# Kernel optimization log

Hardware: AMD Instinct MI355X
Metric: run time of the kernel (lower is better)

Reference implementation:

```python
import jax, jax.numpy as jnp
import numpy as np

D_MODEL = 1024
NUM_HEADS = 16
HEAD_DIM = D_MODEL // NUM_HEADS


def setup_inputs() -> dict:
    key = jax.random.key(0)
    k0, k1, k2, k3, k4 = jax.random.split(key, 5)
    B, S, D = 4, 2048, D_MODEL
    std = np.sqrt(2.0 / (D + D)).astype(np.float32)
    return {
        "in_features": jax.random.normal(k0, (B, S, D), dtype=jnp.float32),
        "Wq": jax.random.normal(k1, (D, D), dtype=jnp.float32) * std,
        "Wk": jax.random.normal(k2, (D, D), dtype=jnp.float32) * std,
        "Wv": jax.random.normal(k3, (D, D), dtype=jnp.float32) * std,
        "Wo": jax.random.normal(k4, (D, D), dtype=jnp.float32) * std,
    }


def reference(in_features, Wq, Wk, Wv, Wo):
    B, S, D = in_features.shape
    H, Hd = NUM_HEADS, HEAD_DIM

    def split_heads(x):  # (B,S,D) -> (B,H,S,Hd)
        return x.reshape(B, S, H, Hd).transpose(0, 2, 1, 3)

    q = split_heads(in_features @ Wq.T)
    k = split_heads(in_features @ Wk.T)
    v = split_heads(in_features @ Wv.T)

    scale = 1.0 / jnp.sqrt(jnp.asarray(Hd, dtype=q.dtype))
    scores = jnp.einsum("bhsd,bhtd->bhst", q, k) * scale  # (B,H,S,S)
    causal = jnp.tril(jnp.ones((S, S), dtype=bool))  # (S,S)
    scores = jnp.where(causal[None, None], scores, -jnp.inf)
    attn = jax.nn.softmax(scores, axis=-1)
    out = jnp.einsum("bhst,bhtd->bhsd", attn, v)  # (B,H,S,Hd)
    out = out.transpose(0, 2, 1, 3).reshape(B, S, D)
    return out @ Wo.T
```

## Files before the change

### kernel.cpp

```cpp
#include <hip/hip_runtime.h>


typedef float f32x4 __attribute__((ext_vector_type(4)));
typedef float f32x16 __attribute__((ext_vector_type(16)));
typedef short s16x8 __attribute__((ext_vector_type(8)));

#if __has_builtin(__builtin_amdgcn_exp2f)
#define EXP2(x) __builtin_amdgcn_exp2f(x)
#else
#define EXP2(x) exp2f(x)
#endif

__device__ __forceinline__ unsigned short f2bf(float f) {
  unsigned int u = __float_as_uint(f);
  u += 0x7fffu + ((u >> 16) & 1u);
  return (unsigned short)(u >> 16);
}

__device__ __forceinline__ unsigned int pk2bf(float f0, float f1) {
  return __builtin_amdgcn_perm(__float_as_uint(f1) + 0x8000u,
                               __float_as_uint(f0) + 0x8000u, 0x07060302u);
}

__device__ __forceinline__ unsigned int pk2bf_t(float f0, float f1) {
  return __builtin_amdgcn_perm(__float_as_uint(f1), __float_as_uint(f0), 0x07060302u);
}

__device__ __forceinline__ void gl_lds16(const short* g, short* lds) {
  __builtin_amdgcn_global_load_lds(
      (const __attribute__((address_space(1))) unsigned int*)g,
      (__attribute__((address_space(3))) unsigned int*)lds, 16, 0, 0);
}

__global__ __launch_bounds__(256) void cvt_all(const float4* __restrict__ X,
                                               const float4* __restrict__ Wq,
                                               const float4* __restrict__ Wk,
                                               const float4* __restrict__ Wv,
                                               const float4* __restrict__ Wo,
                                               ushort4* __restrict__ xb,
                                               ushort4* __restrict__ wqkv,
                                               ushort4* __restrict__ wob) {
  const int NX = 8192 * 1024 / 4;
  const int NW = 1024 * 1024 / 4;
  const int NT = NX + 4 * NW;
  int i = blockIdx.x * blockDim.x + threadIdx.x;
  int stride = gridDim.x * blockDim.x;
  for (int idx = i; idx < NT; idx += stride) {
    const float4* s;
    ushort4* d;
    int off;
    if (idx < NX) {
      s = X; d = xb; off = idx;
    } else {
      int j = idx - NX;
      int w = j >> 18;
      off = j & (NW - 1);
      switch (w) {
        case 0: s = Wq; d = wqkv; break;
        case 1: s = Wk; d = wqkv + NW; break;
        case 2: s = Wv; d = wqkv + 2 * NW; break;
        default: s = Wo; d = wob; break;
      }
    }
    float4 f = s[off];
    ushort4 r;
    r.x = f2bf(f.x); r.y = f2bf(f.y); r.z = f2bf(f.z); r.w = f2bf(f.w);
    d[off] = r;
  }
}

template <int MODE>
__global__ __launch_bounds__(256) void gemm_bt(const short* __restrict__ A,
                                               const short* __restrict__ B,
                                               float* __restrict__ Cf,
                                               short* __restrict__ q_o,
                                               short* __restrict__ k_o,
                                               short* __restrict__ vT_o,
                                               int M, int N, int K) {
  const int tid = threadIdx.x;
  const int wave = tid >> 6, lane = tid & 63;
  const int quad = lane >> 4, l15 = lane & 15;
  const int m0 = blockIdx.x * 128, n0 = blockIdx.y * 128;
  const int wm = (wave >> 1) * 64, wn = (wave & 1) * 64;

  __shared__ __align__(16) short As[128 * 64];
  __shared__ __align__(16) short Bs[128 * 64];

  const f32x4 z4 = {0.f, 0.f, 0.f, 0.f};
  f32x4 acc[4][4];
  for (int i = 0; i < 4; ++i)
    for (int j = 0; j < 4; ++j) acc[i][j] = z4;

  for (int k0 = 0; k0 < K; k0 += 64) {
    __syncthreads();
    for (int i = 0; i < 4; ++i) {
      int c = wave * 4 + i;
      int r = c * 8 + (lane >> 3);
      int c8 = (lane & 7) ^ (r & 7);
      gl_lds16(A + (size_t)(m0 + r) * K + k0 + c8 * 8, As + c * 512 + lane * 8);
      gl_lds16(B + (size_t)(n0 + r) * K + k0 + c8 * 8, Bs + c * 512 + lane * 8);
    }
    __syncthreads();
    for (int kk = 0; kk < 64; kk += 32) {
      int c8b = (kk >> 3) + quad;
      s16x8 af[4], bfr[4];
      for (int mt = 0; mt < 4; ++mt) {
        int row = wm + mt * 16 + l15;
        af[mt] = *(const s16x8*)(As + row * 64 + ((c8b ^ (row & 7)) << 3));
      }
      for (int nt = 0; nt < 4; ++nt) {
        int row = wn + nt * 16 + l15;
        bfr[nt] = *(const s16x8*)(Bs + row * 64 + ((c8b ^ (row & 7)) << 3));
      }
      for (int mt = 0; mt < 4; ++mt)
        for (int nt = 0; nt < 4; ++nt)
          acc[mt][nt] = __builtin_amdgcn_mfma_f32_16x16x32_bf16(af[mt], bfr[nt],
                                                                acc[mt][nt], 0, 0, 0);
    }
  }

  if (MODE == 0) {
    for (int mt = 0; mt < 4; ++mt)
      for (int nt = 0; nt < 4; ++nt) {
        int col = n0 + wn + nt * 16 + l15;
        for (int r = 0; r < 4; ++r) {
          int row = m0 + wm + mt * 16 + quad * 4 + r;
          Cf[(size_t)row * N + col] = acc[mt][nt][r];
        }
      }
  } else {
    if (n0 < 1024) {
      const float scale = 0.18033688011112042f;
      for (int mt = 0; mt < 4; ++mt)
        for (int nt = 0; nt < 4; ++nt) {
          int col = n0 + wn + nt * 16 + l15;
          for (int r = 0; r < 4; ++r) {
            int row = m0 + wm + mt * 16 + quad * 4 + r;
            ((unsigned short*)q_o)[(size_t)row * 1024 + col] = f2bf(acc[mt][nt][r] * scale);
          }
        }
    } else if (n0 < 2048) {
      for (int mt = 0; mt < 4; ++mt)
        for (int nt = 0; nt < 4; ++nt) {
          int col = n0 - 1024 + wn + nt * 16 + l15;
          for (int r = 0; r < 4; ++r) {
            int row = m0 + wm + mt * 16 + quad * 4 + r;
            ((unsigned short*)k_o)[(size_t)row * 1024 + col] = f2bf(acc[mt][nt][r]);
          }
        }
    } else {
      for (int mt = 0; mt < 4; ++mt)
        for (int nt = 0; nt < 4; ++nt) {
          int col = n0 - 2048 + wn + nt * 16 + l15;
          int h = col >> 6, d = col & 63;
          int row0 = m0 + wm + mt * 16 + quad * 4;
          int b = row0 >> 11, s = row0 & 2047;
          uint2 pk;
          pk.x = pk2bf(acc[mt][nt][0], acc[mt][nt][1]);
          pk.y = pk2bf(acc[mt][nt][2], acc[mt][nt][3]);
          *(uint2*)((unsigned short*)vT_o + (((size_t)b * 16 + h) * 64 + d) * 2048 + s) = pk;
        }
    }
  }
}

__global__ __launch_bounds__(256, 2) void attn_kernel(const short* __restrict__ qb,
                                                      const short* __restrict__ kb,
                                                      const short* __restrict__ vT,
                                                      short* __restrict__ ob) {
  const int bh = blockIdx.x;
  const int qt = 15 - (int)blockIdx.y;
  const int tid = threadIdx.x;
  const int wave = tid >> 6, lane = tid & 63;
  const int l31 = lane & 31, h = lane >> 5;
  const int q0 = qt * 128;
  const size_t rowbase = (size_t)(bh >> 4) * 2048;
  const int hoff = (bh & 15) * 64;

  __shared__ __align__(16) short Ks[2][8192];
  __shared__ __align__(16) short VTs[2][8192];

  const int kc = wave * 4;
  const int kr = kc * 8 + (lane >> 3);
  const short* ksrc = kb + (rowbase + kr) * 1024 + hoff + (((lane & 7) ^ (kr & 7)) << 3);
  const int vg = lane & 15;
  const short* vsrc_i[4];
#pragma unroll
  for (int i = 0; i < 4; ++i) {
    int d = (kc + i) * 4 + (lane >> 4);
    vsrc_i[i] = vT + ((size_t)bh * 64 + d) * 2048 + ((vg ^ (d & 7)) << 3);
  }

  s16x8 qf[4];
  {
    const short* qrow = qb + (rowbase + q0 + wave * 32 + l31) * 1024 + hoff + h * 8;
#pragma unroll
    for (int k = 0; k < 4; ++k) qf[k] = *(const s16x8*)(qrow + k * 16);
  }

#pragma unroll
  for (int i = 0; i < 4; ++i)
    gl_lds16(ksrc + i * 8 * 1024, Ks[0] + (kc + i) * 512 + lane * 8);
#pragma unroll
  for (int i = 0; i < 4; ++i)
    gl_lds16(vsrc_i[i], VTs[0] + (kc + i) * 512 + lane * 8);

  f32x16 oacc[2];
#pragma unroll
  for (int dt = 0; dt < 2; ++dt)
#pragma unroll
    for (int e = 0; e < 16; ++e) oacc[dt][e] = 0.f;
  float lacc = 0.f;
  const int kswz = l31 & 7;

  for (int t = 0; t <= qt; ++t) {
    __syncthreads();
    const int cur = t & 1;

    if (t < qt) {
      const int nxt = cur ^ 1;
      const short* ks = ksrc + (size_t)(t + 1) * 128 * 1024;
#pragma unroll
      for (int i = 0; i < 4; ++i)
        gl_lds16(ks + i * 8 * 1024, Ks[nxt] + (kc + i) * 512 + lane * 8);
#pragma unroll
      for (int i = 0; i < 4; ++i)
        gl_lds16(vsrc_i[i] + (t + 1) * 128, VTs[nxt] + (kc + i) * 512 + lane * 8);
    }

    const short* Kc = Ks[cur];
    const short* Vc = VTs[cur];

    unsigned int pp[4][8];
    float sum = 0.f;
#pragma unroll
    for (int g = 0; g < 2; ++g) {
      f32x16 s0, s1;
#pragma unroll
      for (int e = 0; e < 16; ++e) { s0[e] = 0.f; s1[e] = 0.f; }
      __builtin_amdgcn_s_setprio(1);
#pragma unroll
      for (int ks = 0; ks < 4; ++ks) {
        int pos = ((ks << 1) + h) ^ kswz;
        s16x8 kf0 = *(const s16x8*)(Kc + ((2 * g) * 32 + l31) * 64 + (pos << 3));
        s16x8 kf1 = *(const s16x8*)(Kc + ((2 * g + 1) * 32 + l31) * 64 + (pos << 3));
        s0 = __builtin_amdgcn_mfma_f32_32x32x16_bf16(kf0, qf[ks], s0, 0, 0, 0);
        s1 = __builtin_amdgcn_mfma_f32_32x32x16_bf16(kf1, qf[ks], s1, 0, 0, 0);
      }
      __builtin_amdgcn_s_setprio(0);
      if (t == qt) {
        int qg = wave * 32 + l31;
#pragma unroll
        for (int e = 0; e < 16; ++e) {
          int rloc = (e & 3) + 8 * (e >> 2) + 4 * h;
          if ((2 * g) * 32 + rloc > qg) s0[e] = -1e30f;
          if ((2 * g + 1) * 32 + rloc > qg) s1[e] = -1e30f;
        }
      }
#pragma unroll
      for (int rg = 0; rg < 8; ++rg) {
        float a0 = EXP2(s0[2 * rg]), a1 = EXP2(s0[2 * rg + 1]);
        float b0 = EXP2(s1[2 * rg]), b1 = EXP2(s1[2 * rg + 1]);
        sum += (a0 + a1) + (b0 + b1);
        pp[2 * g][rg] = pk2bf_t(a0, a1);
        pp[2 * g + 1][rg] = pk2bf_t(b0, b1);
      }
    }
    lacc += sum;

#pragma unroll
    for (int s = 0; s < 8; ++s) {
      int m = s >> 1, base = (s & 1) * 4;
      unsigned int cax = pp[m][base + 0], cay = pp[m][base + 1];
      unsigned int cbx = pp[m][base + 2], cby = pp[m][base + 3];
      asm("v_permlane32_swap_b32 %0, %1" : "+v"(cax), "+v"(cbx));
      asm("v_permlane32_swap_b32 %0, %1" : "+v"(cay), "+v"(cby));
      union { s16x8 v; unsigned int u[4]; } pf;
      pf.u[0] = cax;
      pf.u[1] = cay;
      pf.u[2] = cbx;
      pf.u[3] = cby;
      __builtin_amdgcn_s_setprio(1);
#pragma unroll
      for (int dt = 0; dt < 2; ++dt) {
        int d = dt * 32 + l31;
        s16x8 vf = *(const s16x8*)(Vc + d * 128 + ((((s << 1) + h) ^ (d & 7)) << 3));
        oacc[dt] = __builtin_amdgcn_mfma_f32_32x32x16_bf16(vf, pf.v, oacc[dt], 0, 0, 0);
      }
      __builtin_amdgcn_s_setprio(0);
    }
  }

  lacc += __shfl_xor(lacc, 32);
  float inv = 1.0f / lacc;
  size_t row = rowbase + q0 + wave * 32 + l31;
  unsigned short* orow = (unsigned short*)ob + row * 1024 + hoff;
#pragma unroll
  for (int dt = 0; dt < 2; ++dt)
#pragma unroll
    for (int rg = 0; rg < 4; ++rg) {
      int d = dt * 32 + rg * 8 + 4 * h;
      uint2 pk;
      pk.x = pk2bf(oacc[dt][rg * 4 + 0] * inv, oacc[dt][rg * 4 + 1] * inv);
      pk.y = pk2bf(oacc[dt][rg * 4 + 2] * inv, oacc[dt][rg * 4 + 3] * inv);
      *(uint2*)(orow + d) = pk;
    }
}

extern "C" void kernel_launch(void* const* d_in, const int* in_sizes, int n_in,
                              void* d_out, int out_size, void* d_ws, size_t ws_size,
                              hipStream_t stream) {
  const float* X  = (const float*)d_in[0];
  const float* Wq = (const float*)d_in[1];
  const float* Wk = (const float*)d_in[2];
  const float* Wv = (const float*)d_in[3];
  const float* Wo = (const float*)d_in[4];

  short* xb   = (short*)d_ws;
  short* wqkv = xb + (size_t)8192 * 1024;
  short* wob  = wqkv + (size_t)3072 * 1024;
  short* qb   = wob + (size_t)1024 * 1024;
  short* kb   = qb + (size_t)8192 * 1024;
  short* vT   = kb + (size_t)8192 * 1024;
  short* ob   = xb;

  const int MB = 8192;

  cvt_all<<<3072, 256, 0, stream>>>((const float4*)X, (const float4*)Wq, (const float4*)Wk,
                                    (const float4*)Wv, (const float4*)Wo, (ushort4*)xb,
                                    (ushort4*)wqkv, (ushort4*)wob);

  gemm_bt<1><<<dim3(64, 24), 256, 0, stream>>>(xb, wqkv, nullptr, qb, kb, vT, MB, 3072, 1024);

  attn_kernel<<<dim3(64, 16), 256, 0, stream>>>(qb, kb, vT, ob);

  gemm_bt<0><<<dim3(64, 8), 256, 0, stream>>>(ob, wob, (float*)d_out, nullptr, nullptr,
                                              nullptr, MB, 1024, 1024);
}
```

Before: 232.0 us.

## Restructure attention to 2 waves each owning 64 query rows with 64-key tiles

```diff
diff --git a/kernel.cpp b/kernel.cpp
--- a/kernel.cpp
+++ b/kernel.cpp
@@ -164,7 +164,7 @@
   }
 }
 
-__global__ __launch_bounds__(256, 2) void attn_kernel(const short* __restrict__ qb,
+__global__ __launch_bounds__(128, 2) void attn_kernel(const short* __restrict__ qb,
                                                       const short* __restrict__ kb,
                                                       const short* __restrict__ vT,
                                                       short* __restrict__ ob) {
@@ -177,25 +177,29 @@
   const size_t rowbase = (size_t)(bh >> 4) * 2048;
   const int hoff = (bh & 15) * 64;
 
-  __shared__ __align__(16) short Ks[2][8192];
-  __shared__ __align__(16) short VTs[2][8192];
+  __shared__ __align__(16) short Ks[2][4096];
+  __shared__ __align__(16) short VTs[2][4096];
 
   const int kc = wave * 4;
   const int kr = kc * 8 + (lane >> 3);
   const short* ksrc = kb + (rowbase + kr) * 1024 + hoff + (((lane & 7) ^ (kr & 7)) << 3);
-  const int vg = lane & 15;
+  const int vg = lane & 7;
   const short* vsrc_i[4];
 #pragma unroll
   for (int i = 0; i < 4; ++i) {
-    int d = (kc + i) * 4 + (lane >> 4);
+    int d = (kc + i) * 8 + (lane >> 3);
     vsrc_i[i] = vT + ((size_t)bh * 64 + d) * 2048 + ((vg ^ (d & 7)) << 3);
   }
 
-  s16x8 qf[4];
+  s16x8 qfA[4], qfB[4];
   {
-    const short* qrow = qb + (rowbase + q0 + wave * 32 + l31) * 1024 + hoff + h * 8;
-#pragma unroll
-    for (int k = 0; k < 4; ++k) qf[k] = *(const s16x8*)(qrow + k * 16);
+    const short* qrowA = qb + (rowbase + q0 + wave * 64 + l31) * 1024 + hoff + h * 8;
+    const short* qrowB = qrowA + 32 * 1024;
+#pragma unroll
+    for (int k = 0; k < 4; ++k) {
+      qfA[k] = *(const s16x8*)(qrowA + k * 16);
+      qfB[k] = *(const s16x8*)(qrowB + k * 16);
+    }
   }
 
 #pragma unroll
@@ -205,105 +209,122 @@
   for (int i = 0; i < 4; ++i)
     gl_lds16(vsrc_i[i], VTs[0] + (kc + i) * 512 + lane * 8);
 
-  f32x16 oacc[2];
+  f32x16 oaccA[2], oaccB[2];
 #pragma unroll
   for (int dt = 0; dt < 2; ++dt)
 #pragma unroll
-    for (int e = 0; e < 16; ++e) oacc[dt][e] = 0.f;
-  float lacc = 0.f;
+    for (int e = 0; e < 16; ++e) { oaccA[dt][e] = 0.f; oaccB[dt][e] = 0.f; }
+  float laccA = 0.f, laccB = 0.f;
   const int kswz = l31 & 7;
-
-  for (int t = 0; t <= qt; ++t) {
+  const int TT = 2 * qt + 1;
+  const int myT = 2 * qt + wave;
+
+  for (int t = 0; t <= TT; ++t) {
     __syncthreads();
     const int cur = t & 1;
 
-    if (t < qt) {
+    if (t < TT) {
       const int nxt = cur ^ 1;
-      const short* ks = ksrc + (size_t)(t + 1) * 128 * 1024;
+      const short* ks = ksrc + (size_t)(t + 1) * 64 * 1024;
 #pragma unroll
       for (int i = 0; i < 4; ++i)
         gl_lds16(ks + i * 8 * 1024, Ks[nxt] + (kc + i) * 512 + lane * 8);
 #pragma unroll
       for (int i = 0; i < 4; ++i)
-        gl_lds16(vsrc_i[i] + (t + 1) * 128, VTs[nxt] + (kc + i) * 512 + lane * 8);
-    }
+        gl_lds16(vsrc_i[i] + (t + 1) * 64, VTs[nxt] + (kc + i) * 512 + lane * 8);
+    }
+
+    if (t > myT) continue;
 
     const short* Kc = Ks[cur];
     const short* Vc = VTs[cur];
 
-    unsigned int pp[4][8];
-    float sum = 0.f;
-#pragma unroll
-    for (int g = 0; g < 2; ++g) {
-      f32x16 s0, s1;
-#pragma unroll
-      for (int e = 0; e < 16; ++e) { s0[e] = 0.f; s1[e] = 0.f; }
+    unsigned int ppA[2][8], ppB[2][8];
+    float sumA = 0.f, sumB = 0.f;
+    {
+      f32x16 sA0, sA1, sB0, sB1;
+#pragma unroll
+      for (int e = 0; e < 16; ++e) { sA0[e] = 0.f; sA1[e] = 0.f; sB0[e] = 0.f; sB1[e] = 0.f; }
       __builtin_amdgcn_s_setprio(1);
 #pragma unroll
       for (int ks = 0; ks < 4; ++ks) {
         int pos = ((ks << 1) + h) ^ kswz;
-        s16x8 kf0 = *(const s16x8*)(Kc + ((2 * g) * 32 + l31) * 64 + (pos << 3));
-        s16x8 kf1 = *(const s16x8*)(Kc + ((2 * g + 1) * 32 + l31) * 64 + (pos << 3));
-        s0 = __builtin_amdgcn_mfma_f32_32x32x16_bf16(kf0, qf[ks], s0, 0, 0, 0);
-        s1 = __builtin_amdgcn_mfma_f32_32x32x16_bf16(kf1, qf[ks], s1, 0, 0, 0);
+        s16x8 kf0 = *(const s16x8*)(Kc + (l31) * 64 + (pos << 3));
+        s16x8 kf1 = *(const s16x8*)(Kc + (32 + l31) * 64 + (pos << 3));
+        sA0 = __builtin_amdgcn_mfma_f32_32x32x16_bf16(kf0, qfA[ks], sA0, 0, 0, 0);
+        sB0 = __builtin_amdgcn_mfma_f32_32x32x16_bf16(kf0, qfB[ks], sB0, 0, 0, 0);
+        sA1 = __builtin_amdgcn_mfma_f32_32x32x16_bf16(kf1, qfA[ks], sA1, 0, 0, 0);
+        sB1 = __builtin_amdgcn_mfma_f32_32x32x16_bf16(kf1, qfB[ks], sB1, 0, 0, 0);
       }
       __builtin_amdgcn_s_setprio(0);
-      if (t == qt) {
-        int qg = wave * 32 + l31;
+      if (t == myT) {
 #pragma unroll
         for (int e = 0; e < 16; ++e) {
           int rloc = (e & 3) + 8 * (e >> 2) + 4 * h;
-          if ((2 * g) * 32 + rloc > qg) s0[e] = -1e30f;
-          if ((2 * g + 1) * 32 + rloc > qg) s1[e] = -1e30f;
+          if (rloc > l31) { sA0[e] = -1e30f; sB1[e] = -1e30f; }
+          sA1[e] = -1e30f;
         }
       }
 #pragma unroll
       for (int rg = 0; rg < 8; ++rg) {
-        float a0 = EXP2(s0[2 * rg]), a1 = EXP2(s0[2 * rg + 1]);
-        float b0 = EXP2(s1[2 * rg]), b1 = EXP2(s1[2 * rg + 1]);
-        sum += (a0 + a1) + (b0 + b1);
-        pp[2 * g][rg] = pk2bf_t(a0, a1);
-        pp[2 * g + 1][rg] = pk2bf_t(b0, b1);
-      }
-    }
-    lacc += sum;
-
-#pragma unroll
-    for (int s = 0; s < 8; ++s) {
+        float a0 = EXP2(sA0[2 * rg]), a1 = EXP2(sA0[2 * rg + 1]);
+        float a2 = EXP2(sA1[2 * rg]), a3 = EXP2(sA1[2 * rg + 1]);
+        float b0 = EXP2(sB0[2 * rg]), b1 = EXP2(sB0[2 * rg + 1]);
+        float b2 = EXP2(sB1[2 * rg]), b3 = EXP2(sB1[2 * rg + 1]);
+        sumA += (a0 + a1) + (a2 + a3);
+        sumB += (b0 + b1) + (b2 + b3);
+        ppA[0][rg] = pk2bf_t(a0, a1);
+        ppA[1][rg] = pk2bf_t(a2, a3);
+        ppB[0][rg] = pk2bf_t(b0, b1);
+        ppB[1][rg] = pk2bf_t(b2, b3);
+      }
+    }
+    laccA += sumA; laccB += sumB;
+
+#pragma unroll
+    for (int s = 0; s < 4; ++s) {
       int m = s >> 1, base = (s & 1) * 4;
-      unsigned int cax = pp[m][base + 0], cay = pp[m][base + 1];
-      unsigned int cbx = pp[m][base + 2], cby = pp[m][base + 3];
-      asm("v_permlane32_swap_b32 %0, %1" : "+v"(cax), "+v"(cbx));
-      asm("v_permlane32_swap_b32 %0, %1" : "+v"(cay), "+v"(cby));
-      union { s16x8 v; unsigned int u[4]; } pf;
-      pf.u[0] = cax;
-      pf.u[1] = cay;
-      pf.u[2] = cbx;
-      pf.u[3] = cby;
+      unsigned int aAx = ppA[m][base + 0], aAy = ppA[m][base + 1];
+      unsigned int bAx = ppA[m][base + 2], bAy = ppA[m][base + 3];
+      asm("v_permlane32_swap_b32 %0, %1" : "+v"(aAx), "+v"(bAx));
+      asm("v_permlane32_swap_b32 %0, %1" : "+v"(aAy), "+v"(bAy));
+      unsigned int aBx = ppB[m][base + 0], aBy = ppB[m][base + 1];
+      unsigned int bBx = ppB[m][base + 2], bBy = ppB[m][base + 3];
+      asm("v_permlane32_swap_b32 %0, %1" : "+v"(aBx), "+v"(bBx));
+      asm("v_permlane32_swap_b32 %0, %1" : "+v"(aBy), "+v"(bBy));
+      union { s16x8 v; unsigned int u[4]; } pfA, pfB;
+      pfA.u[0] = aAx; pfA.u[1] = aAy; pfA.u[2] = bAx; pfA.u[3] = bAy;
+      pfB.u[0] = aBx; pfB.u[1] = aBy; pfB.u[2] = bBx; pfB.u[3] = bBy;
       __builtin_amdgcn_s_setprio(1);
 #pragma unroll
       for (int dt = 0; dt < 2; ++dt) {
         int d = dt * 32 + l31;
-        s16x8 vf = *(const s16x8*)(Vc + d * 128 + ((((s << 1) + h) ^ (d & 7)) << 3));
-        oacc[dt] = __builtin_amdgcn_mfma_f32_32x32x16_bf16(vf, pf.v, oacc[dt], 0, 0, 0);
+        s16x8 vf = *(const s16x8*)(Vc + d * 64 + ((((s << 1) + h) ^ (d & 7)) << 3));
+        oaccA[dt] = __builtin_amdgcn_mfma_f32_32x32x16_bf16(vf, pfA.v, oaccA[dt], 0, 0, 0);
+        oaccB[dt] = __builtin_amdgcn_mfma_f32_32x32x16_bf16(vf, pfB.v, oaccB[dt], 0, 0, 0);
       }
       __builtin_amdgcn_s_setprio(0);
     }
   }
 
-  lacc += __shfl_xor(lacc, 32);
-  float inv = 1.0f / lacc;
-  size_t row = rowbase + q0 + wave * 32 + l31;
-  unsigned short* orow = (unsigned short*)ob + row * 1024 + hoff;
+  laccA += __shfl_xor(laccA, 32);
+  laccB += __shfl_xor(laccB, 32);
+  float invA = 1.0f / laccA, invB = 1.0f / laccB;
+  size_t rowA = rowbase + q0 + wave * 64 + l31;
+  unsigned short* orowA = (unsigned short*)ob + rowA * 1024 + hoff;
+  unsigned short* orowB = orowA + 32 * 1024;
 #pragma unroll
   for (int dt = 0; dt < 2; ++dt)
 #pragma unroll
     for (int rg = 0; rg < 4; ++rg) {
       int d = dt * 32 + rg * 8 + 4 * h;
-      uint2 pk;
-      pk.x = pk2bf(oacc[dt][rg * 4 + 0] * inv, oacc[dt][rg * 4 + 1] * inv);
-      pk.y = pk2bf(oacc[dt][rg * 4 + 2] * inv, oacc[dt][rg * 4 + 3] * inv);
-      *(uint2*)(orow + d) = pk;
+      uint2 pkA, pkB;
+      pkA.x = pk2bf(oaccA[dt][rg * 4 + 0] * invA, oaccA[dt][rg * 4 + 1] * invA);
+      pkA.y = pk2bf(oaccA[dt][rg * 4 + 2] * invA, oaccA[dt][rg * 4 + 3] * invA);
+      pkB.x = pk2bf(oaccB[dt][rg * 4 + 0] * invB, oaccB[dt][rg * 4 + 1] * invB);
+      pkB.y = pk2bf(oaccB[dt][rg * 4 + 2] * invB, oaccB[dt][rg * 4 + 3] * invB);
+      *(uint2*)(orowA + d) = pkA;
+      *(uint2*)(orowB + d) = pkB;
     }
 }
 
@@ -332,7 +353,7 @@
 
   gemm_bt<1><<<dim3(64, 24), 256, 0, stream>>>(xb, wqkv, nullptr, qb, kb, vT, MB, 3072, 1024);
 
-  attn_kernel<<<dim3(64, 16), 256, 0, stream>>>(qb, kb, vT, ob);
+  attn_kernel<<<dim3(64, 16), 128, 0, stream>>>(qb, kb, vT, ob);
 
   gemm_bt<0><<<dim3(64, 8), 256, 0, stream>>>(ob, wob, (float*)d_out, nullptr, nullptr,
                                               nullptr, MB, 1024, 1024);
```

Result: slower. 241.9 us, median of 2 (+4.3%).
